# Performance work log

Hardware: AMD Instinct MI355X
Metric: run time of the kernel (lower is better)

The kernel has to match this reference:

```python
import jax, jax.numpy as jnp
import numpy as np

B, T, D, H = 2, 2048, 2048, 16
HD = D // H  # 128


def _rope_tables(t, hd):
    # standard RoPE frequencies
    inv_freq = 1.0 / (10000.0 ** (np.arange(0, hd, 2, dtype=np.float32) / hd))
    pos = np.arange(t, dtype=np.float32)
    freqs = np.outer(pos, inv_freq)          # [t, hd/2]
    emb = np.concatenate([freqs, freqs], -1)  # [t, hd]
    return jnp.asarray(np.cos(emb)), jnp.asarray(np.sin(emb))


def setup_inputs() -> dict:
    key = jax.random.key(0)
    k1, k2, k3 = jax.random.split(key, 3)
    x = jax.random.normal(k1, (B, T, D), dtype=jnp.float32)
    cos, sin = _rope_tables(T, HD)
    Wqkv = jax.random.normal(k2, (3 * D, D), dtype=jnp.float32) * (D ** -0.5)
    Wout = jax.random.normal(k3, (D, D), dtype=jnp.float32) * (D ** -0.5)
    return {"x": x, "cos": cos, "sin": sin, "Wqkv": Wqkv, "Wout": Wout}


def _rotate_half(u):
    u1, u2 = jnp.split(u, 2, axis=-1)
    return jnp.concatenate([-u2, u1], axis=-1)


def _apply_rotary(u, cos, sin):
    # u: [b,h,t,hd]; cos/sin: [t,hd] broadcast over b,h
    return u * cos[None, None] + _rotate_half(u) * sin[None, None]


def reference(x, cos, sin, Wqkv, Wout):
    b, t, d = x.shape
    qkv = jnp.einsum('btd,ed->bte', x, Wqkv)                 # [b,t,3d]
    qkv = qkv.reshape(b, t, 3, H, HD).transpose(2, 0, 3, 1, 4)  # [3,b,h,t,hd]
    q, k, v = qkv[0], qkv[1], qkv[2]
    q = _apply_rotary(q, cos, sin)
    k = _apply_rotary(k, cos, sin)
    scale = 1.0 / jnp.sqrt(jnp.asarray(HD, dtype=x.dtype))
    scores = jnp.einsum('bhqe,bhke->bhqk', q, k) * scale      # [b,h,t,t]
    causal = jnp.tril(jnp.ones((t, t), dtype=bool))
    scores = jnp.where(causal[None, None], scores, jnp.asarray(-jnp.inf, dtype=scores.dtype))
    probs = jax.nn.softmax(scores, axis=-1)
    attn = jnp.einsum('bhqk,bhke->bhqe', probs, v)            # [b,h,t,hd]
    attn = attn.transpose(0, 2, 1, 3).reshape(b, t, d)
    return jnp.einsum('btd,ed->bte', attn, Wout)
```

## Files before the change

### kernel.cpp

```cpp
#include <hip/hip_runtime.h>
#include <hip/hip_bf16.h>
#include <stdint.h>

#define T_SEQ 2048
#define D_MODEL 2048
#define N_HEADS 16
#define HEAD_DIM 128

typedef __hip_bfloat16 bf16_t;
typedef __attribute__((ext_vector_type(8))) short short8;
typedef __attribute__((ext_vector_type(4))) short short4v;
typedef __attribute__((ext_vector_type(4))) float f32x4;

__device__ __forceinline__ unsigned short f2bf(float x) {
  union { float f; unsigned u; } c; c.f = x;
  unsigned u = c.u;
  u += 0x7fffu + ((u >> 16) & 1u);
  return (unsigned short)(u >> 16);
}
__device__ __forceinline__ float bf2f(short v) {
  union { unsigned u; float f; } c;
  c.u = ((unsigned)(unsigned short)v) << 16;
  return c.f;
}
__device__ __forceinline__ void async16(const bf16_t* g, bf16_t* l) {
  __builtin_amdgcn_global_load_lds(
      (const __attribute__((address_space(1))) void*)g,
      (__attribute__((address_space(3))) void*)l, 16, 0, 0);
}

__global__ __launch_bounds__(256) void cvt_kernel(const float* __restrict__ in,
                                                  unsigned short* __restrict__ out,
                                                  int n4) {
  int i = blockIdx.x * 256 + threadIdx.x;
  if (i >= n4) return;
  float4 v = ((const float4*)in)[i];
  short4v o;
  o[0] = (short)f2bf(v.x); o[1] = (short)f2bf(v.y);
  o[2] = (short)f2bf(v.z); o[3] = (short)f2bf(v.w);
  ((short4v*)out)[i] = o;
}

template<int F32OUT>
__global__ __launch_bounds__(512, 4) void gemm_tp_kernel(
    const bf16_t* __restrict__ A, const bf16_t* __restrict__ Bm,
    float* __restrict__ Cf, unsigned short* __restrict__ Cb,
    int M, int N, int K, int nbn) {
  __shared__ bf16_t lds[36864];
  const int tid = threadIdx.x;
  const int w = tid >> 6, lane = tid & 63;
  const int wm = w >> 2, wn = w & 3;
  const int l15 = lane & 15, g = lane >> 4;

  const int nwg = gridDim.x;
  const int cpx = nwg >> 3;
  const int wg = (blockIdx.x & 7) * cpx + (blockIdx.x >> 3);
  const int bm0 = (wg / nbn) * 128, bn0 = (wg % nbn) * 256;

  const int sl = tid >> 3;
  const int su = (tid & 7) ^ (sl & 7);
  const int srow = (sl << 1) | (su >> 2);
  const int sc8 = su & 3;
  const bf16_t* agA = A + (size_t)(bm0 + srow) * K + sc8 * 8;
  const bf16_t* agB = Bm + (size_t)(bn0 + srow) * K + sc8 * 8;

#define STAGE(KT, SB) do {                                                    \
    bf16_t* _d = lds + (SB) * 12288 + w * 512;         \
    async16(agA + (size_t)(KT) * 32, _d);                                     \
    async16(agB + (size_t)(KT) * 32, _d + 4096);                              \
    async16(agB + 128 * (size_t)K + (size_t)(KT) * 32, _d + 8192);            \
  } while (0)

  const int lhalf = l15 >> 1;
  const int aoff = lhalf * 64 + (((((l15 & 1) << 2) | g) ^ lhalf)) * 8;
  const bf16_t* Abase = lds + wm * 2048 + aoff;
  const bf16_t* Bbase = lds + 4096 + wn * 2048 + aoff;

  f32x4 acc[4][4];
#pragma unroll
  for (int i = 0; i < 4; ++i)
#pragma unroll
    for (int j = 0; j < 4; ++j)
#pragma unroll
      for (int e = 0; e < 4; ++e) acc[i][j][e] = 0.0f;

  STAGE(0, 0);
  STAGE(1, 1);

  const int NT = K >> 5;
  int cb = 0, sb = 2;
  for (int kt = 0; kt < NT - 1; ++kt) {
    asm volatile("s_waitcnt vmcnt(3)" ::: "memory");
    __builtin_amdgcn_s_barrier();
    const bf16_t* Ab = Abase + cb * 12288;
    const bf16_t* Bb = Bbase + cb * 12288;
    short8 af[4], bfr[4];
#pragma unroll
    for (int mi = 0; mi < 4; ++mi) af[mi] = *(const short8*)(Ab + mi * 512);
#pragma unroll
    for (int ni = 0; ni < 4; ++ni) bfr[ni] = *(const short8*)(Bb + ni * 512);
    if (kt < NT - 2) STAGE(kt + 2, sb);
    __builtin_amdgcn_s_setprio(1);
#pragma unroll
    for (int mi = 0; mi < 4; ++mi)
#pragma unroll
      for (int ni = 0; ni < 4; ++ni)
        acc[mi][ni] = __builtin_amdgcn_mfma_f32_16x16x32_bf16(
            af[mi], bfr[ni], acc[mi][ni], 0, 0, 0);
    __builtin_amdgcn_s_setprio(0);
    cb = (cb == 2) ? 0 : cb + 1;
    sb = (sb == 2) ? 0 : sb + 1;
  }
  {
    asm volatile("s_waitcnt vmcnt(0)" ::: "memory");
    __builtin_amdgcn_s_barrier();
    const bf16_t* Ab = Abase + cb * 12288;
    const bf16_t* Bb = Bbase + cb * 12288;
    short8 af[4], bfr[4];
#pragma unroll
    for (int mi = 0; mi < 4; ++mi) af[mi] = *(const short8*)(Ab + mi * 512);
#pragma unroll
    for (int ni = 0; ni < 4; ++ni) bfr[ni] = *(const short8*)(Bb + ni * 512);
    __builtin_amdgcn_s_setprio(1);
#pragma unroll
    for (int mi = 0; mi < 4; ++mi)
#pragma unroll
      for (int ni = 0; ni < 4; ++ni)
        acc[mi][ni] = __builtin_amdgcn_mfma_f32_16x16x32_bf16(
            af[mi], bfr[ni], acc[mi][ni], 0, 0, 0);
    __builtin_amdgcn_s_setprio(0);
  }
#undef STAGE

#pragma unroll
  for (int mi = 0; mi < 4; ++mi)
#pragma unroll
    for (int ni = 0; ni < 4; ++ni)
#pragma unroll
      for (int r = 0; r < 4; ++r) {
        int mr = bm0 + wm * 64 + mi * 16 + g * 4 + r;
        int nc = bn0 + wn * 64 + ni * 16 + l15;
        if (F32OUT)
          Cf[(size_t)mr * N + nc] = acc[mi][ni][r];
        else
          Cb[(size_t)mr * N + nc] = f2bf(acc[mi][ni][r]);
      }
}

__global__ __launch_bounds__(256) void rope_kernel(
    const bf16_t* __restrict__ qkv,
    const float* __restrict__ cosb, const float* __restrict__ sinb,
    bf16_t* __restrict__ qo, bf16_t* __restrict__ ko, bf16_t* __restrict__ vT) {
  const int nTT = T_SEQ / 64;
  const int bx = blockIdx.x;
  const int bh = bx / nTT, tt = bx % nTT;
  const int b = bh / N_HEADS, h = bh % N_HEADS;
  const int tid = threadIdx.x;
  __shared__ bf16_t vlds[64][136];

  const float SC = 0.08838834764831845f;

#pragma unroll
  for (int it = 0; it < 2; ++it) {
    int item = it * 256 + tid;
    int r = item >> 3, cg = item & 7;
    int t = tt * 64 + r;
    int c0 = cg * 8;
    size_t base = ((size_t)b * T_SEQ + t) * (size_t)(3 * D_MODEL) + (size_t)h * HEAD_DIM;

    float cs0[8], sn0[8], cs1[8], sn1[8];
    {
      const float* cp = cosb + (size_t)t * HEAD_DIM + c0;
      const float* sp = sinb + (size_t)t * HEAD_DIM + c0;
      float4 a0 = *(const float4*)(cp), a1 = *(const float4*)(cp + 4);
      float4 b0 = *(const float4*)(cp + 64), b1 = *(const float4*)(cp + 68);
      float4 s0 = *(const float4*)(sp), s1 = *(const float4*)(sp + 4);
      float4 t0 = *(const float4*)(sp + 64), t1 = *(const float4*)(sp + 68);
      cs0[0]=a0.x; cs0[1]=a0.y; cs0[2]=a0.z; cs0[3]=a0.w; cs0[4]=a1.x; cs0[5]=a1.y; cs0[6]=a1.z; cs0[7]=a1.w;
      cs1[0]=b0.x; cs1[1]=b0.y; cs1[2]=b0.z; cs1[3]=b0.w; cs1[4]=b1.x; cs1[5]=b1.y; cs1[6]=b1.z; cs1[7]=b1.w;
      sn0[0]=s0.x; sn0[1]=s0.y; sn0[2]=s0.z; sn0[3]=s0.w; sn0[4]=s1.x; sn0[5]=s1.y; sn0[6]=s1.z; sn0[7]=s1.w;
      sn1[0]=t0.x; sn1[1]=t0.y; sn1[2]=t0.z; sn1[3]=t0.w; sn1[4]=t1.x; sn1[5]=t1.y; sn1[6]=t1.z; sn1[7]=t1.w;
    }

#pragma unroll
    for (int sec = 0; sec < 2; ++sec) {
      size_t sbase = base + (size_t)sec * D_MODEL;
      short8 lo = *(const short8*)(qkv + sbase + c0);
      short8 hi = *(const short8*)(qkv + sbase + 64 + c0);
      short8 olo, ohi;
#pragma unroll
      for (int e = 0; e < 8; ++e) {
        float xl = bf2f(lo[e]), xh = bf2f(hi[e]);
        float rl = xl * cs0[e] - xh * sn0[e];
        float rh = xh * cs1[e] + xl * sn1[e];
        if (sec == 0) { rl *= SC; rh *= SC; }
        olo[e] = (short)f2bf(rl);
        ohi[e] = (short)f2bf(rh);
      }
      bf16_t* dst = (sec == 0 ? qo : ko) + ((size_t)bh * T_SEQ + t) * HEAD_DIM + c0;
      *(short8*)dst = olo;
      *(short8*)(dst + 64) = ohi;
    }

    short8 v0 = *(const short8*)(qkv + base + 2 * D_MODEL + c0);
    short8 v1 = *(const short8*)(qkv + base + 2 * D_MODEL + 64 + c0);
    *(short8*)&vlds[r][c0] = v0;
    *(short8*)&vlds[r][64 + c0] = v1;
  }
  __syncthreads();

  int hd = tid >> 1, hf = tid & 1;
  bf16_t* dst = vT + ((size_t)bh * HEAD_DIM + hd) * T_SEQ + tt * 64 + hf * 32;
#pragma unroll
  for (int jj = 0; jj < 4; ++jj) {
    short8 o;
#pragma unroll
    for (int e = 0; e < 8; ++e)
      o[e] = *(const short*)&vlds[hf * 32 + jj * 8 + e][hd];
    *(short8*)(dst + jj * 8) = o;
  }
}

__global__ __launch_bounds__(256) void attn_kernel(
    const bf16_t* __restrict__ q, const bf16_t* __restrict__ k,
    const bf16_t* __restrict__ vT, unsigned short* __restrict__ attn) {
  const int bx = blockIdx.x;
  const int bh = bx & 31;
  const int qt = 31 - (bx >> 5);
  const int b = bh / N_HEADS, h = bh % N_HEADS;
  const int tid = threadIdx.x;
  const int w = tid >> 6, lane = tid & 63;
  const int l15 = lane & 15, g = lane >> 4;
  const float LOG2E = 1.44269504088896340736f;

  __shared__ bf16_t Ks[2][64 * 128];
  __shared__ bf16_t Vs[2][128 * 64];
  __shared__ bf16_t plds[4][16][72];

  const bf16_t* qb = q + (size_t)bh * T_SEQ * HEAD_DIM;
  const bf16_t* kb = k + (size_t)bh * T_SEQ * HEAD_DIM;
  const bf16_t* vb = vT + (size_t)bh * HEAD_DIM * T_SEQ;

  const int qrow = qt * 64 + w * 16 + l15;
  short8 qf[4];
#pragma unroll
  for (int kk = 0; kk < 4; ++kk)
    qf[kk] = *(const short8*)(qb + (size_t)qrow * HEAD_DIM + kk * 32 + g * 8);

  float m[4], l[4];
  f32x4 acc[8];
#pragma unroll
  for (int r = 0; r < 4; ++r) { m[r] = -3.0e38f; l[r] = 0.0f; }
#pragma unroll
  for (int fh = 0; fh < 8; ++fh)
#pragma unroll
    for (int e = 0; e < 4; ++e) acc[fh][e] = 0.0f;

#define STAGE_TILES(KT, BU)                                                      \
  {                                                                              \
    _Pragma("unroll")                                                            \
    for (int j = 0; j < 4; ++j) {                                                \
      int s = j * 4 + w;                                                         \
      int row = s * 4 + (lane >> 4);                                             \
      int gc = (lane & 15) ^ (row & 7);                                          \
      async16(kb + (size_t)((KT) * 64 + row) * HEAD_DIM + gc * 8,                \
              &Ks[BU][s * 512]);                                                 \
    }                                                                            \
    _Pragma("unroll")                                                            \
    for (int j = 0; j < 4; ++j) {                                                \
      int s = j * 4 + w;                                                         \
      int row = s * 8 + (lane >> 3);                                             \
      int gc = (lane & 7) ^ (row & 7);                                           \
      async16(vb + (size_t)row * T_SEQ + (KT) * 64 + gc * 8,                     \
              &Vs[BU][s * 512]);                                                 \
    }                                                                            \
  }

  STAGE_TILES(0, 0);
  __syncthreads();
  int buf = 0;

  for (int kt = 0; kt <= qt; ++kt) {
    if (kt < qt) STAGE_TILES(kt + 1, buf ^ 1);

    f32x4 s[4];
#pragma unroll
    for (int f = 0; f < 4; ++f)
#pragma unroll
      for (int e = 0; e < 4; ++e) s[f][e] = 0.0f;
    __builtin_amdgcn_s_setprio(1);
#pragma unroll
    for (int f = 0; f < 4; ++f) {
      int row = f * 16 + l15;
      int r7 = l15 & 7;
#pragma unroll
      for (int kk = 0; kk < 4; ++kk) {
        short8 kf = *(const short8*)(&Ks[buf][row * 128 + (((kk * 4 + g) ^ r7) << 3)]);
        s[f] = __builtin_amdgcn_mfma_f32_16x16x32_bf16(qf[kk], kf, s[f], 0, 0, 0);
      }
    }
    __builtin_amdgcn_s_setprio(0);

    if (kt == qt) {
#pragma unroll
      for (int f = 0; f < 4; ++f) {
        int kv = f * 16 + l15;
#pragma unroll
        for (int r = 0; r < 4; ++r) {
          int qq = w * 16 + g * 4 + r;
          if (kv > qq) s[f][r] = -3.0e38f;
        }
      }
    }
    float rmax[4];
#pragma unroll
    for (int r = 0; r < 4; ++r)
      rmax[r] = fmaxf(fmaxf(s[0][r], s[1][r]), fmaxf(s[2][r], s[3][r]));
#pragma unroll
    for (int off = 1; off < 16; off <<= 1)
#pragma unroll
      for (int r = 0; r < 4; ++r)
        rmax[r] = fmaxf(rmax[r], __shfl_xor(rmax[r], off, 64));

    float fac[4], rsum[4];
#pragma unroll
    for (int r = 0; r < 4; ++r) {
      float mn = fmaxf(m[r], rmax[r]);
      fac[r] = exp2f((m[r] - mn) * LOG2E);
      m[r] = mn;
      rsum[r] = 0.0f;
    }
#pragma unroll
    for (int f = 0; f < 4; ++f)
#pragma unroll
      for (int r = 0; r < 4; ++r) {
        float pv = exp2f((s[f][r] - m[r]) * LOG2E);
        s[f][r] = pv;
        rsum[r] += pv;
      }
#pragma unroll
    for (int off = 1; off < 16; off <<= 1)
#pragma unroll
      for (int r = 0; r < 4; ++r)
        rsum[r] += __shfl_xor(rsum[r], off, 64);
#pragma unroll
    for (int r = 0; r < 4; ++r) l[r] = l[r] * fac[r] + rsum[r];
#pragma unroll
    for (int fh = 0; fh < 8; ++fh)
#pragma unroll
      for (int r = 0; r < 4; ++r) acc[fh][r] *= fac[r];

#pragma unroll
    for (int f = 0; f < 4; ++f)
#pragma unroll
      for (int r = 0; r < 4; ++r)
        *(unsigned short*)&plds[w][g * 4 + r][f * 16 + l15] = f2bf(s[f][r]);

    short8 pf0 = *(const short8*)&plds[w][l15][g * 8];
    short8 pf1 = *(const short8*)&plds[w][l15][32 + g * 8];

    __builtin_amdgcn_s_setprio(1);
#pragma unroll
    for (int fh = 0; fh < 8; ++fh) {
      int row = fh * 16 + l15;
      int r7 = l15 & 7;
      short8 vf0 = *(const short8*)(&Vs[buf][row * 64 + ((g ^ r7) << 3)]);
      short8 vf1 = *(const short8*)(&Vs[buf][row * 64 + (((4 + g) ^ r7) << 3)]);
      acc[fh] = __builtin_amdgcn_mfma_f32_16x16x32_bf16(pf0, vf0, acc[fh], 0, 0, 0);
      acc[fh] = __builtin_amdgcn_mfma_f32_16x16x32_bf16(pf1, vf1, acc[fh], 0, 0, 0);
    }
    __builtin_amdgcn_s_setprio(0);

    __syncthreads();
    buf ^= 1;
  }

  float inv[4];
#pragma unroll
  for (int r = 0; r < 4; ++r) inv[r] = 1.0f / l[r];
#pragma unroll
  for (int fh = 0; fh < 8; ++fh)
#pragma unroll
    for (int r = 0; r < 4; ++r) {
      int tg = qt * 64 + w * 16 + g * 4 + r;
      attn[((size_t)b * T_SEQ + tg) * D_MODEL + (size_t)h * HEAD_DIM + fh * 16 + l15] =
          f2bf(acc[fh][r] * inv[r]);
    }
}

extern "C" void kernel_launch(void* const* d_in, const int* in_sizes, int n_in,
                              void* d_out, int out_size, void* d_ws, size_t ws_size,
                              hipStream_t stream) {
  const float* x    = (const float*)d_in[0];
  const float* cosb = (const float*)d_in[1];
  const float* sinb = (const float*)d_in[2];
  const float* Wqkv = (const float*)d_in[3];
  const float* Wout = (const float*)d_in[4];
  float* out = (float*)d_out;

  char* ws = (char*)d_ws;
  size_t off = 0;
  bf16_t* xb    = (bf16_t*)(ws + off); off += (size_t)4096 * 2048 * 2;
  bf16_t* wqkvb = (bf16_t*)(ws + off); off += (size_t)6144 * 2048 * 2;
  bf16_t* woutb = (bf16_t*)(ws + off); off += (size_t)2048 * 2048 * 2;
  bf16_t* qkvb  = (bf16_t*)(ws + off); off += (size_t)4096 * 6144 * 2;
  bf16_t* qb    = (bf16_t*)(ws + off); off += (size_t)32 * 2048 * 128 * 2;
  bf16_t* kb    = (bf16_t*)(ws + off); off += (size_t)32 * 2048 * 128 * 2;
  bf16_t* vTb   = (bf16_t*)(ws + off); off += (size_t)32 * 2048 * 128 * 2;
  bf16_t* attnb = xb;

  cvt_kernel<<<8192, 256, 0, stream>>>(x, (unsigned short*)xb, 4096 * 2048 / 4);
  cvt_kernel<<<12288, 256, 0, stream>>>(Wqkv, (unsigned short*)wqkvb, 6144 * 2048 / 4);
  cvt_kernel<<<4096, 256, 0, stream>>>(Wout, (unsigned short*)woutb, 2048 * 2048 / 4);

  gemm_tp_kernel<0><<<768, 512, 0, stream>>>(xb, wqkvb, nullptr, (unsigned short*)qkvb,
                                             4096, 6144, 2048, 24);

  rope_kernel<<<1024, 256, 0, stream>>>(qkvb, cosb, sinb, qb, kb, vTb);

  attn_kernel<<<1024, 256, 0, stream>>>(qb, kb, vTb, (unsigned short*)attnb);

  gemm_tp_kernel<1><<<256, 512, 0, stream>>>(attnb, woutb, out, nullptr,
                                             4096, 2048, 2048, 8);
}
```

Baseline: 297.7 us.

## Rework attention to 128-row query tiles with 32x32 MFMA and register P exchange

The attention kernel now gives each workgroup 128 query rows (32 per wave) instead of 64, halving the grid to 512 blocks. It switches from 16x16x32 to 32x32x16 MFMA, computing S transposed so the softmax reduction needs only one cross-half shuffle. P is converted to bf16 with packed cvt and exchanged through lane shuffles instead of an LDS round trip. The output is staged in LDS so global stores are coalesced 16-byte writes. Causal block ordering is changed to pair long and short tiles. The intent is to reuse each K/V tile across more query rows and cut shuffle and LDS traffic, at the cost of higher register pressure and fewer blocks.

```diff
diff --git a/kernel.cpp b/kernel.cpp
--- a/kernel.cpp
+++ b/kernel.cpp
@@ -11,6 +11,7 @@
 typedef __attribute__((ext_vector_type(8))) short short8;
 typedef __attribute__((ext_vector_type(4))) short short4v;
 typedef __attribute__((ext_vector_type(4))) float f32x4;
+typedef __attribute__((ext_vector_type(16))) float f32x16;
 
 __device__ __forceinline__ unsigned short f2bf(float x) {
   union { float f; unsigned u; } c; c.f = x;
@@ -65,7 +66,7 @@
   const bf16_t* agB = Bm + (size_t)(bn0 + srow) * K + sc8 * 8;
 
 #define STAGE(KT, SB) do {                                                    \
-    bf16_t* _d = lds + (SB) * 12288 + w * 512;         \
+    bf16_t* _d = lds + (SB) * 12288 + w * 512;                                \
     async16(agA + (size_t)(KT) * 32, _d);                                     \
     async16(agB + (size_t)(KT) * 32, _d + 4096);                              \
     async16(agB + 128 * (size_t)K + (size_t)(KT) * 32, _d + 8192);            \
@@ -221,50 +222,50 @@
   }
 }
 
-__global__ __launch_bounds__(256) void attn_kernel(
+__global__ __launch_bounds__(256, 2) void attn_kernel(
     const bf16_t* __restrict__ q, const bf16_t* __restrict__ k,
     const bf16_t* __restrict__ vT, unsigned short* __restrict__ attn) {
   const int bx = blockIdx.x;
   const int bh = bx & 31;
-  const int qt = 31 - (bx >> 5);
+  const int qi = (bx >> 5) & 7;
+  const int qt = (bx >> 8) ? qi : 15 - qi;
   const int b = bh / N_HEADS, h = bh % N_HEADS;
   const int tid = threadIdx.x;
   const int w = tid >> 6, lane = tid & 63;
-  const int l15 = lane & 15, g = lane >> 4;
+  const int l31 = lane & 31, hi = lane >> 5;
+  const int swz = l31 & 7;
   const float LOG2E = 1.44269504088896340736f;
 
-  __shared__ bf16_t Ks[2][64 * 128];
-  __shared__ bf16_t Vs[2][128 * 64];
-  __shared__ bf16_t plds[4][16][72];
+  __shared__ bf16_t smem[32768];
 
   const bf16_t* qb = q + (size_t)bh * T_SEQ * HEAD_DIM;
   const bf16_t* kb = k + (size_t)bh * T_SEQ * HEAD_DIM;
   const bf16_t* vb = vT + (size_t)bh * HEAD_DIM * T_SEQ;
 
-  const int qrow = qt * 64 + w * 16 + l15;
-  short8 qf[4];
-#pragma unroll
-  for (int kk = 0; kk < 4; ++kk)
-    qf[kk] = *(const short8*)(qb + (size_t)qrow * HEAD_DIM + kk * 32 + g * 8);
-
-  float m[4], l[4];
-  f32x4 acc[8];
-#pragma unroll
-  for (int r = 0; r < 4; ++r) { m[r] = -3.0e38f; l[r] = 0.0f; }
-#pragma unroll
-  for (int fh = 0; fh < 8; ++fh)
-#pragma unroll
-    for (int e = 0; e < 4; ++e) acc[fh][e] = 0.0f;
-
-#define STAGE_TILES(KT, BU)                                                      \
-  {                                                                              \
+  const int qlo = qt * 128 + w * 32;
+  const int qhi = qlo + 31;
+  const int qrow = qlo + l31;
+
+  short8 qf[8];
+#pragma unroll
+  for (int ks = 0; ks < 8; ++ks)
+    qf[ks] = *(const short8*)(qb + (size_t)qrow * HEAD_DIM + ks * 16 + hi * 8);
+
+  float m = -3.0e38f, l = 0.0f;
+  f32x16 O[4];
+#pragma unroll
+  for (int dt = 0; dt < 4; ++dt)
+#pragma unroll
+    for (int r = 0; r < 16; ++r) O[dt][r] = 0.0f;
+
+#define STAGE_TILES(KT, BU) {                                                    \
     _Pragma("unroll")                                                            \
     for (int j = 0; j < 4; ++j) {                                                \
       int s = j * 4 + w;                                                         \
       int row = s * 4 + (lane >> 4);                                             \
       int gc = (lane & 15) ^ (row & 7);                                          \
       async16(kb + (size_t)((KT) * 64 + row) * HEAD_DIM + gc * 8,                \
-              &Ks[BU][s * 512]);                                                 \
+              smem + (BU) * 8192 + s * 512);                                     \
     }                                                                            \
     _Pragma("unroll")                                                            \
     for (int j = 0; j < 4; ++j) {                                                \
@@ -272,7 +273,7 @@
       int row = s * 8 + (lane >> 3);                                             \
       int gc = (lane & 7) ^ (row & 7);                                           \
       async16(vb + (size_t)row * T_SEQ + (KT) * 64 + gc * 8,                     \
-              &Vs[BU][s * 512]);                                                 \
+              smem + 16384 + (BU) * 8192 + s * 512);                             \
     }                                                                            \
   }
 
@@ -280,112 +281,134 @@
   __syncthreads();
   int buf = 0;
 
-  for (int kt = 0; kt <= qt; ++kt) {
-    if (kt < qt) STAGE_TILES(kt + 1, buf ^ 1);
-
-    f32x4 s[4];
-#pragma unroll
-    for (int f = 0; f < 4; ++f)
-#pragma unroll
-      for (int e = 0; e < 4; ++e) s[f][e] = 0.0f;
-    __builtin_amdgcn_s_setprio(1);
-#pragma unroll
-    for (int f = 0; f < 4; ++f) {
-      int row = f * 16 + l15;
-      int r7 = l15 & 7;
-#pragma unroll
-      for (int kk = 0; kk < 4; ++kk) {
-        short8 kf = *(const short8*)(&Ks[buf][row * 128 + (((kk * 4 + g) ^ r7) << 3)]);
-        s[f] = __builtin_amdgcn_mfma_f32_16x16x32_bf16(qf[kk], kf, s[f], 0, 0, 0);
-      }
-    }
-    __builtin_amdgcn_s_setprio(0);
-
-    if (kt == qt) {
-#pragma unroll
-      for (int f = 0; f < 4; ++f) {
-        int kv = f * 16 + l15;
-#pragma unroll
-        for (int r = 0; r < 4; ++r) {
-          int qq = w * 16 + g * 4 + r;
-          if (kv > qq) s[f][r] = -3.0e38f;
+  const int lastk = 2 * qt + 1;
+  for (int kt = 0; kt <= lastk; ++kt) {
+    if (kt < lastk) STAGE_TILES(kt + 1, buf ^ 1);
+    const bf16_t* Ks = smem + buf * 8192;
+    const bf16_t* Vs = smem + 16384 + buf * 8192;
+    const bool active = (kt * 64 <= qhi);
+
+    if (active) {
+      f32x16 S[2];
+#pragma unroll
+      for (int kvt = 0; kvt < 2; ++kvt) {
+        const int kvbase = kt * 64 + kvt * 32;
+        if (kvbase <= qhi) {
+          const int krow = kvt * 32 + l31;
+#pragma unroll
+          for (int r = 0; r < 16; ++r) S[kvt][r] = 0.0f;
+          __builtin_amdgcn_s_setprio(1);
+#pragma unroll
+          for (int ks = 0; ks < 8; ++ks) {
+            int c = (2 * ks + hi) ^ swz;
+            short8 kf = *(const short8*)(Ks + krow * 128 + c * 8);
+            S[kvt] = __builtin_amdgcn_mfma_f32_32x32x16_bf16(kf, qf[ks], S[kvt], 0, 0, 0);
+          }
+          __builtin_amdgcn_s_setprio(0);
+          if (kvbase + 31 > qlo) {
+#pragma unroll
+            for (int r = 0; r < 16; ++r) {
+              int kv = kvbase + (r & 3) + 8 * (r >> 2) + 4 * hi;
+              if (kv > qrow) S[kvt][r] = -3.0e38f;
+            }
+          }
+        } else {
+#pragma unroll
+          for (int r = 0; r < 16; ++r) S[kvt][r] = -3.0e38f;
         }
       }
+
+      float rl = -3.0e38f;
+#pragma unroll
+      for (int kvt = 0; kvt < 2; ++kvt)
+#pragma unroll
+        for (int r = 0; r < 16; ++r) rl = fmaxf(rl, S[kvt][r]);
+      rl = fmaxf(rl, __shfl_xor(rl, 32, 64));
+      float mn = fmaxf(m, rl);
+      float fac = exp2f((m - mn) * LOG2E);
+      m = mn;
+      float sum = 0.0f;
+#pragma unroll
+      for (int kvt = 0; kvt < 2; ++kvt)
+#pragma unroll
+        for (int r = 0; r < 16; ++r) {
+          float p = exp2f((S[kvt][r] - m) * LOG2E);
+          S[kvt][r] = p;
+          sum += p;
+        }
+      sum += __shfl_xor(sum, 32, 64);
+      l = l * fac + sum;
+#pragma unroll
+      for (int dt = 0; dt < 4; ++dt)
+#pragma unroll
+        for (int r = 0; r < 16; ++r) O[dt][r] *= fac;
+
+      short8 pf[4];
+#pragma unroll
+      for (int ks = 0; ks < 4; ++ks) {
+        const int kvt = ks >> 1;
+        const int base = (ks & 1) * 8;
+        unsigned pkL0, pkL1, pkH0, pkH1;
+        {
+          float a0 = S[kvt][base + 0], a1 = S[kvt][base + 1];
+          float a2 = S[kvt][base + 2], a3 = S[kvt][base + 3];
+          float b0 = S[kvt][base + 4], b1 = S[kvt][base + 5];
+          float b2 = S[kvt][base + 6], b3 = S[kvt][base + 7];
+          asm("v_cvt_pk_bf16_f32 %0, %1, %2" : "=v"(pkL0) : "v"(a0), "v"(a1));
+          asm("v_cvt_pk_bf16_f32 %0, %1, %2" : "=v"(pkL1) : "v"(a2), "v"(a3));
+          asm("v_cvt_pk_bf16_f32 %0, %1, %2" : "=v"(pkH0) : "v"(b0), "v"(b1));
+          asm("v_cvt_pk_bf16_f32 %0, %1, %2" : "=v"(pkH1) : "v"(b2), "v"(b3));
+        }
+        unsigned sx0 = hi ? pkL0 : pkH0;
+        unsigned sx1 = hi ? pkL1 : pkH1;
+        unsigned rx0 = (unsigned)__shfl_xor((int)sx0, 32, 64);
+        unsigned rx1 = (unsigned)__shfl_xor((int)sx1, 32, 64);
+        union { unsigned u[4]; short8 s; } uu;
+        uu.u[0] = hi ? rx0 : pkL0;
+        uu.u[1] = hi ? rx1 : pkL1;
+        uu.u[2] = hi ? pkH0 : rx0;
+        uu.u[3] = hi ? pkH1 : rx1;
+        pf[ks] = uu.s;
+      }
+
+      __builtin_amdgcn_s_setprio(1);
+#pragma unroll
+      for (int dt = 0; dt < 4; ++dt) {
+        const int vrow = dt * 32 + l31;
+#pragma unroll
+        for (int ks = 0; ks < 4; ++ks) {
+          int c = (2 * ks + hi) ^ swz;
+          short8 vf = *(const short8*)(Vs + vrow * 64 + c * 8);
+          O[dt] = __builtin_amdgcn_mfma_f32_32x32x16_bf16(vf, pf[ks], O[dt], 0, 0, 0);
+        }
+      }
+      __builtin_amdgcn_s_setprio(0);
     }
-    float rmax[4];
-#pragma unroll
-    for (int r = 0; r < 4; ++r)
-      rmax[r] = fmaxf(fmaxf(s[0][r], s[1][r]), fmaxf(s[2][r], s[3][r]));
-#pragma unroll
-    for (int off = 1; off < 16; off <<= 1)
-#pragma unroll
-      for (int r = 0; r < 4; ++r)
-        rmax[r] = fmaxf(rmax[r], __shfl_xor(rmax[r], off, 64));
-
-    float fac[4], rsum[4];
-#pragma unroll
-    for (int r = 0; r < 4; ++r) {
-      float mn = fmaxf(m[r], rmax[r]);
-      fac[r] = exp2f((m[r] - mn) * LOG2E);
-      m[r] = mn;
-      rsum[r] = 0.0f;
-    }
-#pragma unroll
-    for (int f = 0; f < 4; ++f)
-#pragma unroll
-      for (int r = 0; r < 4; ++r) {
-        float pv = exp2f((s[f][r] - m[r]) * LOG2E);
-        s[f][r] = pv;
-        rsum[r] += pv;
-      }
-#pragma unroll
-    for (int off = 1; off < 16; off <<= 1)
-#pragma unroll
-      for (int r = 0; r < 4; ++r)
-        rsum[r] += __shfl_xor(rsum[r], off, 64);
-#pragma unroll
-    for (int r = 0; r < 4; ++r) l[r] = l[r] * fac[r] + rsum[r];
-#pragma unroll
-    for (int fh = 0; fh < 8; ++fh)
-#pragma unroll
-      for (int r = 0; r < 4; ++r) acc[fh][r] *= fac[r];
-
-#pragma unroll
-    for (int f = 0; f < 4; ++f)
-#pragma unroll
-      for (int r = 0; r < 4; ++r)
-        *(unsigned short*)&plds[w][g * 4 + r][f * 16 + l15] = f2bf(s[f][r]);
-
-    short8 pf0 = *(const short8*)&plds[w][l15][g * 8];
-    short8 pf1 = *(const short8*)&plds[w][l15][32 + g * 8];
-
-    __builtin_amdgcn_s_setprio(1);
-#pragma unroll
-    for (int fh = 0; fh < 8; ++fh) {
-      int row = fh * 16 + l15;
-      int r7 = l15 & 7;
-      short8 vf0 = *(const short8*)(&Vs[buf][row * 64 + ((g ^ r7) << 3)]);
-      short8 vf1 = *(const short8*)(&Vs[buf][row * 64 + (((4 + g) ^ r7) << 3)]);
-      acc[fh] = __builtin_amdgcn_mfma_f32_16x16x32_bf16(pf0, vf0, acc[fh], 0, 0, 0);
-      acc[fh] = __builtin_amdgcn_mfma_f32_16x16x32_bf16(pf1, vf1, acc[fh], 0, 0, 0);
-    }
-    __builtin_amdgcn_s_setprio(0);
 
     __syncthreads();
     buf ^= 1;
   }
-
-  float inv[4];
-#pragma unroll
-  for (int r = 0; r < 4; ++r) inv[r] = 1.0f / l[r];
-#pragma unroll
-  for (int fh = 0; fh < 8; ++fh)
-#pragma unroll
-    for (int r = 0; r < 4; ++r) {
-      int tg = qt * 64 + w * 16 + g * 4 + r;
-      attn[((size_t)b * T_SEQ + tg) * D_MODEL + (size_t)h * HEAD_DIM + fh * 16 + l15] =
-          f2bf(acc[fh][r] * inv[r]);
+#undef STAGE_TILES
+
+  float inv = 1.0f / l;
+  bf16_t* ol = smem + w * 4352;
+#pragma unroll
+  for (int dt = 0; dt < 4; ++dt)
+#pragma unroll
+    for (int r = 0; r < 16; ++r) {
+      int d = dt * 32 + (r & 3) + 8 * (r >> 2) + 4 * hi;
+      *(unsigned short*)&ol[l31 * 136 + d] = f2bf(O[dt][r] * inv);
     }
+  __syncthreads();
+  const int srow4 = lane >> 4;
+  const int scol = (lane & 15) * 8;
+#pragma unroll
+  for (int rr = 0; rr < 8; ++rr) {
+    int row = rr * 4 + srow4;
+    short8 v = *(const short8*)(ol + row * 136 + scol);
+    *(short8*)(attn + ((size_t)b * T_SEQ + qt * 128 + w * 32 + row) * D_MODEL +
+               (size_t)h * HEAD_DIM + scol) = v;
+  }
 }
 
 extern "C" void kernel_launch(void* const* d_in, const int* in_sizes, int n_in,
@@ -418,7 +441,7 @@
 
   rope_kernel<<<1024, 256, 0, stream>>>(qkvb, cosb, sinb, qb, kb, vTb);
 
-  attn_kernel<<<1024, 256, 0, stream>>>(qb, kb, vTb, (unsigned short*)attnb);
+  attn_kernel<<<512, 256, 0, stream>>>(qb, kb, vTb, (unsigned short*)attnb);
 
   gemm_tp_kernel<1><<<256, 512, 0, stream>>>(attnb, woutb, out, nullptr,
                                              4096, 2048, 2048, 8);
```

Measured after the change: 274.3 us. 7.8% less time.
